# Kernel tuning notes

Measured on AMD Instinct MI355X. Metric: run time of the kernel, lower is better.

## Reference

```python
import jax, jax.numpy as jnp
import numpy as np

E = 512   # embed_size
H = 8     # heads
D = E // H
WIN = 256 # window_size
N = 4     # batch
S = 2048  # seq len (query_len == key_len == value_len)


def setup_inputs() -> dict:
    key = jax.random.key(0)
    ks = jax.random.split(key, 8)
    s = 0.02
    inp = {
        "value": jax.random.normal(ks[0], (N, S, E), jnp.float32),
        "key":   jax.random.normal(ks[1], (N, S, E), jnp.float32),
        "query": jax.random.normal(ks[2], (N, S, E), jnp.float32),
        "mask":  jnp.ones((N, 1, 1, S), jnp.int32),
        # nn.Linear params: y = x @ W.T + b, W shape [out, in]
        "Wv": jax.random.normal(ks[3], (E, E), jnp.float32) * s,
        "bv": jnp.zeros((E,), jnp.float32),
        "Wk": jax.random.normal(ks[4], (E, E), jnp.float32) * s,
        "bk": jnp.zeros((E,), jnp.float32),
        "Wq": jax.random.normal(ks[5], (E, E), jnp.float32) * s,
        "bq": jnp.zeros((E,), jnp.float32),
        "Wo": jax.random.normal(ks[6], (E, E), jnp.float32) * s,
        "bo": jnp.zeros((E,), jnp.float32),
    }
    return inp


def reference(value, key, query, mask, Wv, bv, Wk, bk, Wq, bq, Wo, bo):
    n, q_len, _ = query.shape
    k_len = key.shape[1]
    w = min(WIN, k_len)  # window_size = min(self.window_size, key_len)

    v = (value @ Wv.T + bv).reshape(n, k_len, H, D)
    k = (key   @ Wk.T + bk).reshape(n, k_len, H, D)
    q = (query @ Wq.T + bq).reshape(n, q_len, H, D)

    # Full QK scores; banded window selected below. Position j is inside the
    # window of query i iff  i - w//2 <= j <= i + w//2 (matches the torch
    # per-i slice [max(0,i-w//2), min(k_len, i+w//2+1)) ).
    scores = jnp.einsum('nqhd,nkhd->nhqk', q, k)  # [N,H,Q,K]
    ii = jnp.arange(q_len)[:, None]
    jj = jnp.arange(k_len)[None, :]
    in_win = (jj >= ii - w // 2) & (jj <= ii + w // 2)  # [Q,K]

    # Inside window: scores, masked to -inf where mask == 0.
    # Outside window: entries stay 0 (the torch code zero-inits attention).
    neg_inf = jnp.float32(-jnp.inf)
    banded = jnp.where(mask != 0, scores, neg_inf)          # broadcast [N,1,1,K]
    att_logits = jnp.where(in_win[None, None], banded, 0.0)  # [N,H,Q,K]

    att_logits = att_logits / jnp.sqrt(jnp.float32(E))  # scale by sqrt(embed_size)
    attention = jax.nn.softmax(att_logits, axis=3)

    out = jnp.einsum('nhqk,nkhd->nqhd', attention, v).reshape(n, q_len, E)
    out = out @ Wo.T + bo
    return (out, attention)
```

## Files before the change

### kernel.cpp

```cpp
#include <hip/hip_runtime.h>


typedef unsigned short u16;
typedef __bf16 bf16x8 __attribute__((ext_vector_type(8)));
typedef float  f32x4  __attribute__((ext_vector_type(4)));
typedef u16    u16x8  __attribute__((ext_vector_type(8)));

#define GLOAD_LDS(gsrc, ldst)                                                  \
    __builtin_amdgcn_global_load_lds(                                          \
        (const __attribute__((address_space(1))) void*)(gsrc),                 \
        (__attribute__((address_space(3))) void*)(ldst), 16, 0, 0)

__device__ __forceinline__ u16 f2bf(float f) {
    union { float f; unsigned u; } x; x.f = f;
    unsigned u = x.u;
    u += 0x7fffu + ((u >> 16) & 1u);
    return (u16)(u >> 16);
}

struct CvtWArgs {
    const float* src[4];
    u16*         dst[4];
};

__global__ __launch_bounds__(256) void cvt_w(CvtWArgs a) {
    int t = blockIdx.x >> 8, blk = blockIdx.x & 255;
    int i = (blk * 256 + threadIdx.x) * 4;
    float4 v = *(const float4*)(a.src[t] + i);
    ushort4 o;
    o.x = f2bf(v.x); o.y = f2bf(v.y); o.z = f2bf(v.z); o.w = f2bf(v.w);
    *(ushort4*)(a.dst[t] + i) = o;
}

__global__ __launch_bounds__(256) void gemm_qkv(
    const float* __restrict__ A0, const float* __restrict__ A1, const float* __restrict__ A2,
    const u16* __restrict__ B,
    const float* __restrict__ b0, const float* __restrict__ b1, const float* __restrict__ b2,
    u16* __restrict__ o0, u16* __restrict__ o1, u16* __restrict__ o2,
    float* __restrict__ sumv)
{
    __shared__ __attribute__((aligned(16))) u16 As[128 * 64];
    __shared__ __attribute__((aligned(16))) u16 Bs[128 * 64];

    const int tid  = threadIdx.x;
    const int lane = tid & 63;
    const int w    = tid >> 6;
    const int bm   = blockIdx.x, bn = blockIdx.y;
    const int wm   = w >> 1, wn = w & 1;

    const int t = bn >> 2;
    const float* A = (t == 0) ? A0 : (t == 1) ? A1 : A2;
    const float* Ag = A + (size_t)bm * 128 * 512;
    const u16* Bg = B + (size_t)bn * 128 * 512;

    f32x4 acc[4][4];
#pragma unroll
    for (int m = 0; m < 4; ++m)
#pragma unroll
        for (int n = 0; n < 4; ++n) acc[m][n] = 0;

    const int swc = ((lane & 7) ^ (lane >> 3)) * 8;
    const int arow = tid >> 1, ahalf = tid & 1;
    const float* asrc = Ag + (size_t)arow * 512 + ahalf * 32;

    for (int k0 = 0; k0 < 512; k0 += 64) {
        float4 fv[8];
#pragma unroll
        for (int i = 0; i < 8; ++i) fv[i] = *(const float4*)(asrc + k0 + i * 4);
#pragma unroll
        for (int c4 = 0; c4 < 4; ++c4) {
            bf16x8 pk;
#pragma unroll
            for (int e = 0; e < 8; ++e) {
                float f = ((const float*)&fv[c4 * 2])[e];
                pk[e] = (__bf16)f;
            }
            int ch = ahalf * 4 + c4;
            *(bf16x8*)(As + arow * 64 + ((ch ^ (arow & 7)) * 8)) = pk;
        }
#pragma unroll
        for (int i = 0; i < 4; ++i) {
            int g = i * 4 + w;
            GLOAD_LDS(Bg + (size_t)(g * 8 + (lane >> 3)) * 512 + k0 + swc, Bs + g * 512);
        }
        __syncthreads();

#pragma unroll
        for (int s = 0; s < 2; ++s) {
            bf16x8 af[4], bf[4];
            int c = s * 4 + (lane >> 4);
#pragma unroll
            for (int m = 0; m < 4; ++m) {
                int r = wm * 64 + m * 16 + (lane & 15);
                af[m] = *(const bf16x8*)(As + r * 64 + ((c ^ (r & 7)) * 8));
                int r2 = wn * 64 + m * 16 + (lane & 15);
                bf[m] = *(const bf16x8*)(Bs + r2 * 64 + ((c ^ (r2 & 7)) * 8));
            }
#pragma unroll
            for (int m = 0; m < 4; ++m)
#pragma unroll
                for (int n = 0; n < 4; ++n)
                    acc[m][n] = __builtin_amdgcn_mfma_f32_16x16x32_bf16(af[m], bf[n], acc[m][n], 0, 0, 0);
        }
        __syncthreads();
    }

    const float* bias = (t == 0) ? b0 : (t == 1) ? b1 : b2;
    u16* ob = (t == 0) ? o0 : (t == 1) ? o1 : o2;
    const int clbase = (bn & 3) * 128;

#pragma unroll
    for (int m = 0; m < 4; ++m) {
#pragma unroll
        for (int n = 0; n < 4; ++n) {
            int cl = clbase + wn * 64 + n * 16 + (lane & 15);
            float bb = bias[cl];
#pragma unroll
            for (int reg = 0; reg < 4; ++reg) {
                int row = bm * 128 + wm * 64 + m * 16 + (lane >> 4) * 4 + reg;
                ob[(size_t)row * 512 + cl] = f2bf(acc[m][n][reg] + bb);
            }
        }
    }

    if (t == 2) {
        int nb = bm >> 4;
#pragma unroll
        for (int n = 0; n < 4; ++n) {
            float s = 0.f;
#pragma unroll
            for (int m = 0; m < 4; ++m)
#pragma unroll
                for (int reg = 0; reg < 4; ++reg) s += acc[m][n][reg];
            s += __shfl_xor(s, 16, 64);
            s += __shfl_xor(s, 32, 64);
            if (lane < 16) {
                int cl = clbase + wn * 64 + n * 16 + lane;
                atomicAdd(sumv + nb * 512 + cl, s);
            }
        }
    }
}

__global__ __launch_bounds__(256) void gemm_o(
    const u16* __restrict__ A, const u16* __restrict__ B,
    const float* __restrict__ bias, float* __restrict__ fo)
{
    __shared__ __attribute__((aligned(16))) u16 As[128 * 64];
    __shared__ __attribute__((aligned(16))) u16 Bs[64 * 64];

    const int tid  = threadIdx.x;
    const int lane = tid & 63;
    const int w    = tid >> 6;
    const int bm   = blockIdx.x, bn = blockIdx.y;
    const int wm   = w >> 1, wn = w & 1;

    const u16* Ag = A + (size_t)bm * 128 * 512;
    const u16* Bg = B + (size_t)bn * 64 * 512;

    f32x4 acc[4][2];
#pragma unroll
    for (int m = 0; m < 4; ++m) { acc[m][0] = 0; acc[m][1] = 0; }

    const int swc = ((lane & 7) ^ (lane >> 3)) * 8;

    for (int k0 = 0; k0 < 512; k0 += 64) {
#pragma unroll
        for (int i = 0; i < 4; ++i) {
            int g = i * 4 + w;
            GLOAD_LDS(Ag + (size_t)(g * 8 + (lane >> 3)) * 512 + k0 + swc, As + g * 512);
        }
#pragma unroll
        for (int i = 0; i < 2; ++i) {
            int g = i * 4 + w;
            GLOAD_LDS(Bg + (size_t)(g * 8 + (lane >> 3)) * 512 + k0 + swc, Bs + g * 512);
        }
        __syncthreads();

#pragma unroll
        for (int s = 0; s < 2; ++s) {
            bf16x8 af[4], bf[2];
            int c = s * 4 + (lane >> 4);
#pragma unroll
            for (int m = 0; m < 4; ++m) {
                int r = wm * 64 + m * 16 + (lane & 15);
                af[m] = *(const bf16x8*)(As + r * 64 + ((c ^ (r & 7)) * 8));
            }
#pragma unroll
            for (int n = 0; n < 2; ++n) {
                int r2 = wn * 32 + n * 16 + (lane & 15);
                bf[n] = *(const bf16x8*)(Bs + r2 * 64 + ((c ^ (r2 & 7)) * 8));
            }
#pragma unroll
            for (int m = 0; m < 4; ++m)
#pragma unroll
                for (int n = 0; n < 2; ++n)
                    acc[m][n] = __builtin_amdgcn_mfma_f32_16x16x32_bf16(af[m], bf[n], acc[m][n], 0, 0, 0);
        }
        __syncthreads();
    }

#pragma unroll
    for (int m = 0; m < 4; ++m) {
#pragma unroll
        for (int n = 0; n < 2; ++n) {
            int cl = bn * 64 + wn * 32 + n * 16 + (lane & 15);
            float bb = bias[cl];
#pragma unroll
            for (int reg = 0; reg < 4; ++reg) {
                int row = bm * 128 + wm * 64 + m * 16 + (lane >> 4) * 4 + reg;
                fo[(size_t)row * 512 + cl] = acc[m][n][reg] + bb;
            }
        }
    }
}

__global__ __launch_bounds__(256) void attn_kernel(
    const u16* __restrict__ qb, const u16* __restrict__ kb,
    const u16* __restrict__ vb, const int* __restrict__ mask,
    const float* __restrict__ sumv, float* __restrict__ att,
    u16* __restrict__ oh) {
    __shared__ __attribute__((aligned(16))) char lds[79616];
    u16*   Qs      = (u16*)lds;
    float* stat_m  = (float*)lds;
    float* stat_rd = (float*)(lds + 128);
    float* stat_c  = (float*)(lds + 256);
    float* red     = (float*)(lds + 384);
    float* red2    = (float*)(lds + 640);
    u16*   Ks      = (u16*)(lds + 4096);
    float* Ab32    = (float*)(lds + 4096);
    u16*   Vt      = (u16*)(lds + 4096 + 37632);

    const int tid  = threadIdx.x;
    const int lane = tid & 63;
    const int w    = tid >> 6;
    const int bid0 = blockIdx.x;
    const int bid  = (bid0 & 7) * 256 + (bid0 >> 3);
    const int tile = bid & 63;
    const int h    = (bid >> 6) & 7;
    const int n    = bid >> 9;
    const int i0   = tile * 32;
    const int jlo  = max(0, i0 - 128);
    const float scale = 0.04419417382415922f;

    const size_t base_nh = (size_t)n * 2048 * 512 + h * 64;
    const int lr = lane >> 3;
    const int swg = ((lane & 7) ^ lr) * 8;

    GLOAD_LDS(qb + base_nh + (size_t)(i0 + w * 8 + lr) * 512 + swg, Qs + w * 512);
    for (int p = 0; p < 9; ++p) {
        int g = p * 4 + w;
        int j = min(jlo + g * 8 + lr, 2047);
        GLOAD_LDS(kb + base_nh + (size_t)j * 512 + swg, Ks + g * 512);
    }
    for (int p = 0; p < 9; ++p) {
        int idx = p * 256 + tid;
        int jj = idx >> 3, ch = idx & 7;
        int j = jlo + jj;
        u16x8 tmp = {0, 0, 0, 0, 0, 0, 0, 0};
        if (j < 2048) tmp = *(const u16x8*)(vb + base_nh + (size_t)j * 512 + ch * 8);
        int jc = jj >> 3, jr = jj & 7;
        int pjc = (jc < 32) ? (jc ^ ch) : jc;
#pragma unroll
        for (int r = 0; r < 8; ++r)
            Vt[(ch * 8 + r) * 296 + pjc * 8 + jr] = tmp[r];
    }
    __syncthreads();

    const int rbase = (w & 1) * 16;
    const int cbase = (w >> 1) * 144;
    f32x4 acc[9];
#pragma unroll
    for (int f = 0; f < 9; ++f) acc[f] = 0;

    bf16x8 aq[2];
    {
        int r = rbase + (lane & 15);
#pragma unroll
        for (int ks = 0; ks < 2; ++ks) {
            int kc = ks * 4 + (lane >> 4);
            aq[ks] = *(const bf16x8*)(Qs + r * 64 + ((kc ^ (r & 7)) * 8));
        }
    }
#pragma unroll
    for (int f = 0; f < 9; ++f) {
        int jj = cbase + f * 16 + (lane & 15);
#pragma unroll
        for (int ks = 0; ks < 2; ++ks) {
            int kc = ks * 4 + (lane >> 4);
            bf16x8 bk_ = *(const bf16x8*)(Ks + jj * 64 + ((kc ^ (jj & 7)) * 8));
            acc[f] = __builtin_amdgcn_mfma_f32_16x16x32_bf16(aq[ks], bk_, acc[f], 0, 0, 0);
        }
    }
    __syncthreads();

    const int rowg = (lane >> 4) * 4;
    f32x4 lv[9];
    float mx[4] = {-__builtin_inff(), -__builtin_inff(), -__builtin_inff(), -__builtin_inff()};
#pragma unroll
    for (int f = 0; f < 9; ++f) {
        int jj = cbase + f * 16 + (lane & 15);
        int j = jlo + jj;
        int mk = (j < 2048) ? mask[n * 2048 + j] : 0;
#pragma unroll
        for (int reg = 0; reg < 4; ++reg) {
            int i = i0 + rbase + rowg + reg;
            bool inw = (j >= i - 128) && (j <= i + 128) && (j < 2048);
            float val = (inw && mk != 0) ? acc[f][reg] * scale : -__builtin_inff();
            lv[f][reg] = val;
            mx[reg] = fmaxf(mx[reg], val);
        }
    }
#pragma unroll
    for (int mskk = 1; mskk < 16; mskk <<= 1)
#pragma unroll
        for (int reg = 0; reg < 4; ++reg)
            mx[reg] = fmaxf(mx[reg], __shfl_xor(mx[reg], mskk, 64));
    if ((lane & 15) == 0) {
#pragma unroll
        for (int reg = 0; reg < 4; ++reg) red[w * 16 + rowg + reg] = mx[reg];
    }
    __syncthreads();
    if (tid < 32) {
        int r = tid;
        int wa = (r < 16) ? 0 : 1, rr = r & 15;
        stat_m[r] = fmaxf(fmaxf(red[wa * 16 + rr], red[(wa + 2) * 16 + rr]), 0.0f);
    }
    __syncthreads();

    float m4[4];
#pragma unroll
    for (int reg = 0; reg < 4; ++reg) m4[reg] = stat_m[rbase + rowg + reg];
    float sm[4] = {0, 0, 0, 0};
#pragma unroll
    for (int f = 0; f < 9; ++f)
#pragma unroll
        for (int reg = 0; reg < 4; ++reg)
            sm[reg] += __expf(lv[f][reg] - m4[reg]);
#pragma unroll
    for (int mskk = 1; mskk < 16; mskk <<= 1)
#pragma unroll
        for (int reg = 0; reg < 4; ++reg)
            sm[reg] += __shfl_xor(sm[reg], mskk, 64);
    if ((lane & 15) == 0) {
#pragma unroll
        for (int reg = 0; reg < 4; ++reg) red2[w * 16 + rowg + reg] = sm[reg];
    }
    __syncthreads();
    if (tid < 32) {
        int r = tid, gi = i0 + r;
        int wa = (r < 16) ? 0 : 1, rr = r & 15;
        float s = red2[wa * 16 + rr] + red2[(wa + 2) * 16 + rr];
        int lo = max(0, gi - 128), hi = min(2048, gi + 129);
        float em = __expf(-stat_m[r]);
        float denom = s + (float)(2048 - (hi - lo)) * em;
        float rd = 1.0f / denom;
        stat_rd[r] = rd;
        stat_c[r] = em * rd;
    }
    __syncthreads();

    float rd4[4], c4[4];
#pragma unroll
    for (int reg = 0; reg < 4; ++reg) {
        rd4[reg] = stat_rd[rbase + rowg + reg];
        c4[reg] = stat_c[rbase + rowg + reg];
    }
#pragma unroll
    for (int f = 0; f < 9; ++f) {
        int jj = cbase + f * 16 + (lane & 15);
        int j = jlo + jj;
#pragma unroll
        for (int reg = 0; reg < 4; ++reg) {
            int it = rbase + rowg + reg;
            int i = i0 + it;
            bool inw = (j >= i - 128) && (j <= i + 128) && (j < 2048);
            float e = __expf(lv[f][reg] - m4[reg]);
            Ab32[it * 292 + jj] = inw ? (e * rd4[reg] - c4[reg]) : 0.0f;
        }
    }
    __syncthreads();

    const int rb2 = (w & 1) * 16;
    const int db  = (w >> 1) * 32;
    f32x4 po[2];
    po[0] = 0; po[1] = 0;
#pragma unroll
    for (int ks = 0; ks < 9; ++ks) {
        int kc = ks * 4 + (lane >> 4);
        int it = rb2 + (lane & 15);
        const float* ap = Ab32 + it * 292 + kc * 8;
        float4 alo = *(const float4*)(ap);
        float4 ahi = *(const float4*)(ap + 4);
        bf16x8 af;
        af[0] = (__bf16)alo.x; af[1] = (__bf16)alo.y;
        af[2] = (__bf16)alo.z; af[3] = (__bf16)alo.w;
        af[4] = (__bf16)ahi.x; af[5] = (__bf16)ahi.y;
        af[6] = (__bf16)ahi.z; af[7] = (__bf16)ahi.w;
#pragma unroll
        for (int f = 0; f < 2; ++f) {
            int d = db + f * 16 + (lane & 15);
            int phys = (kc < 32) ? (kc ^ (d >> 3)) : kc;
            bf16x8 bv_ = *(const bf16x8*)(Vt + d * 296 + phys * 8);
            po[f] = __builtin_amdgcn_mfma_f32_16x16x32_bf16(af, bv_, po[f], 0, 0, 0);
        }
    }
    {
        const float* svp = sumv + (size_t)n * 512 + h * 64;
#pragma unroll
        for (int f = 0; f < 2; ++f) {
            int d = db + f * 16 + (lane & 15);
            float sv = svp[d];
#pragma unroll
            for (int reg = 0; reg < 4; ++reg) {
                int it = rb2 + rowg + reg;
                float val = po[f][reg] + stat_c[it] * sv;
                oh[base_nh + (size_t)(i0 + it) * 512 + d] = f2bf(val);
            }
        }
    }

    {
        int jend = min(2048, jlo + 288);
        size_t rowbase = ((size_t)(n * 8 + h) * 2048 + i0) * 2048;
        for (int idx = tid; idx < 32 * 512; idx += 256) {
            int r = idx >> 9, j4 = idx & 511;
            int j = j4 * 4;
            float c = stat_c[r];
            f32x4 v = {c, c, c, c};
            if (j >= jlo && j < jend) {
                const float* ap = Ab32 + r * 292 + (j - jlo);
                v[0] += ap[0]; v[1] += ap[1]; v[2] += ap[2]; v[3] += ap[3];
            }
            __builtin_nontemporal_store(v, (f32x4*)(att + rowbase + (size_t)r * 2048 + j));
        }
    }
}

extern "C" void kernel_launch(void* const* d_in, const int* in_sizes, int n_in,
                              void* d_out, int out_size, void* d_ws, size_t ws_size,
                              hipStream_t stream) {
    const float* value = (const float*)d_in[0];
    const float* key_  = (const float*)d_in[1];
    const float* query = (const float*)d_in[2];
    const int*   mask  = (const int*)d_in[3];
    const float* Wv = (const float*)d_in[4];
    const float* bv = (const float*)d_in[5];
    const float* Wk = (const float*)d_in[6];
    const float* bk = (const float*)d_in[7];
    const float* Wq = (const float*)d_in[8];
    const float* bq = (const float*)d_in[9];
    const float* Wo = (const float*)d_in[10];
    const float* bo = (const float*)d_in[11];

    char* ws = (char*)d_ws;
    size_t off = 0;
    auto carve = [&](size_t bytes) -> char* {
        char* p = ws + off;
        off += (bytes + 255) & ~(size_t)255;
        return p;
    };
    const size_t XB = (size_t)8192 * 512 * 2;
    const size_t WB = (size_t)512 * 512 * 2;
    u16* wqkv = (u16*)carve(3 * WB);
    u16* wob  = (u16*)carve(WB);
    u16* qb   = (u16*)carve(XB);
    u16* kb   = (u16*)carve(XB);
    u16* vb2  = (u16*)carve(XB);
    u16* ohb  = (u16*)carve(XB);
    float* sumv = (float*)carve(2048 * sizeof(float));

    (void)hipMemsetAsync(sumv, 0, 2048 * sizeof(float), stream);

    CvtWArgs ca;
    ca.src[0] = Wq; ca.dst[0] = wqkv;
    ca.src[1] = Wk; ca.dst[1] = wqkv + (size_t)512 * 512;
    ca.src[2] = Wv; ca.dst[2] = wqkv + (size_t)1024 * 512;
    ca.src[3] = Wo; ca.dst[3] = wob;

    cvt_w<<<dim3(1024), 256, 0, stream>>>(ca);
    gemm_qkv<<<dim3(64, 12), 256, 0, stream>>>(
        query, key_, value, wqkv, bq, bk, bv, qb, kb, vb2, sumv);

    float* att = (float*)d_out + (size_t)4 * 2048 * 512;
    attn_kernel<<<dim3(2048), 256, 0, stream>>>(qb, kb, vb2, mask, sumv, att, ohb);
    gemm_o<<<dim3(64, 8), 256, 0, stream>>>(ohb, wob, bo, (float*)d_out);
}
```

Baseline: 643.6 us.

## Prefetch A tiles in QKV GEMM, split attention-probability stores, fold memset into cvt

The QKV GEMM now reads the next fp32 A tile into registers while MFMAs run on the current tile, and the global loads are laid out in a coalesced row-group pattern. In the attention kernel, the constant out-of-window probability writes are issued as soon as the row stats are known, before the PV matmul, and only the in-window band is written from LDS afterwards. This overlaps the large store traffic with compute. The separate hipMemsetAsync of sumv is folded into the weight-conversion kernel, removing one launch, at the cost of extra register pressure from the prefetch buffer.

```diff
diff --git a/kernel.cpp b/kernel.cpp
--- a/kernel.cpp
+++ b/kernel.cpp
@@ -23,13 +23,16 @@
     u16*         dst[4];
 };
 
-__global__ __launch_bounds__(256) void cvt_w(CvtWArgs a) {
+__global__ __launch_bounds__(256) void cvt_w(CvtWArgs a, float* __restrict__ sumv) {
     int t = blockIdx.x >> 8, blk = blockIdx.x & 255;
     int i = (blk * 256 + threadIdx.x) * 4;
     float4 v = *(const float4*)(a.src[t] + i);
     ushort4 o;
     o.x = f2bf(v.x); o.y = f2bf(v.y); o.z = f2bf(v.z); o.w = f2bf(v.w);
     *(ushort4*)(a.dst[t] + i) = o;
+    if (blockIdx.x == 0) {
+        for (int k = threadIdx.x; k < 2048; k += 256) sumv[k] = 0.f;
+    }
 }
 
 __global__ __launch_bounds__(256) void gemm_qkv(
@@ -60,23 +63,24 @@
         for (int n = 0; n < 4; ++n) acc[m][n] = 0;
 
     const int swc = ((lane & 7) ^ (lane >> 3)) * 8;
-    const int arow = tid >> 1, ahalf = tid & 1;
-    const float* asrc = Ag + (size_t)arow * 512 + ahalf * 32;
+    const int arow_g  = tid >> 4;
+    const int alane16 = tid & 15;
+    const int ach  = alane16 >> 1;
+    const int ahalf = alane16 & 1;
+
+    float4 av[8];
+#pragma unroll
+    for (int p = 0; p < 8; ++p)
+        av[p] = *(const float4*)(Ag + (size_t)(p * 16 + arow_g) * 512 + alane16 * 4);
 
     for (int k0 = 0; k0 < 512; k0 += 64) {
-        float4 fv[8];
-#pragma unroll
-        for (int i = 0; i < 8; ++i) fv[i] = *(const float4*)(asrc + k0 + i * 4);
-#pragma unroll
-        for (int c4 = 0; c4 < 4; ++c4) {
-            bf16x8 pk;
-#pragma unroll
-            for (int e = 0; e < 8; ++e) {
-                float f = ((const float*)&fv[c4 * 2])[e];
-                pk[e] = (__bf16)f;
-            }
-            int ch = ahalf * 4 + c4;
-            *(bf16x8*)(As + arow * 64 + ((ch ^ (arow & 7)) * 8)) = pk;
+#pragma unroll
+        for (int p = 0; p < 8; ++p) {
+            int row = p * 16 + arow_g;
+            ushort4 pk;
+            pk.x = f2bf(av[p].x); pk.y = f2bf(av[p].y);
+            pk.z = f2bf(av[p].z); pk.w = f2bf(av[p].w);
+            *(ushort4*)(As + row * 64 + ((ach ^ (row & 7)) * 8) + ahalf * 4) = pk;
         }
 #pragma unroll
         for (int i = 0; i < 4; ++i) {
@@ -84,6 +88,12 @@
             GLOAD_LDS(Bg + (size_t)(g * 8 + (lane >> 3)) * 512 + k0 + swc, Bs + g * 512);
         }
         __syncthreads();
+
+        if (k0 < 448) {
+#pragma unroll
+            for (int p = 0; p < 8; ++p)
+                av[p] = *(const float4*)(Ag + (size_t)(p * 16 + arow_g) * 512 + (k0 + 64) + alane16 * 4);
+        }
 
 #pragma unroll
         for (int s = 0; s < 2; ++s) {
@@ -241,9 +251,11 @@
     const int n    = bid >> 9;
     const int i0   = tile * 32;
     const int jlo  = max(0, i0 - 128);
+    const int jend = min(2048, jlo + 288);
     const float scale = 0.04419417382415922f;
 
     const size_t base_nh = (size_t)n * 2048 * 512 + h * 64;
+    const size_t rowbase = ((size_t)(n * 8 + h) * 2048 + i0) * 2048;
     const int lr = lane >> 3;
     const int swg = ((lane & 7) ^ lr) * 8;
 
@@ -359,6 +371,17 @@
         stat_c[r] = em * rd;
     }
     __syncthreads();
+
+    {
+        int j4lo = jlo >> 2, j4end = jend >> 2;
+        for (int idx = tid; idx < 32 * 512; idx += 256) {
+            int r = idx >> 9, j4 = idx & 511;
+            if (j4 >= j4lo && j4 < j4end) continue;
+            float c = stat_c[r];
+            f32x4 v = {c, c, c, c};
+            __builtin_nontemporal_store(v, (f32x4*)(att + rowbase + (size_t)r * 2048 + j4 * 4));
+        }
+    }
 
     float rd4[4], c4[4];
 #pragma unroll
@@ -405,6 +428,19 @@
             po[f] = __builtin_amdgcn_mfma_f32_16x16x32_bf16(af, bv_, po[f], 0, 0, 0);
         }
     }
+
+    {
+        int nseg = (jend - jlo) >> 2;
+        for (int idx = tid; idx < 32 * 72; idx += 256) {
+            int r = idx / 72, q = idx % 72;
+            if (q >= nseg) continue;
+            float c = stat_c[r];
+            const float* ap = Ab32 + r * 292 + q * 4;
+            f32x4 v = {ap[0] + c, ap[1] + c, ap[2] + c, ap[3] + c};
+            __builtin_nontemporal_store(v, (f32x4*)(att + rowbase + (size_t)r * 2048 + jlo + q * 4));
+        }
+    }
+
     {
         const float* svp = sumv + (size_t)n * 512 + h * 64;
 #pragma unroll
@@ -417,22 +453,6 @@
                 float val = po[f][reg] + stat_c[it] * sv;
                 oh[base_nh + (size_t)(i0 + it) * 512 + d] = f2bf(val);
             }
-        }
-    }
-
-    {
-        int jend = min(2048, jlo + 288);
-        size_t rowbase = ((size_t)(n * 8 + h) * 2048 + i0) * 2048;
-        for (int idx = tid; idx < 32 * 512; idx += 256) {
-            int r = idx >> 9, j4 = idx & 511;
-            int j = j4 * 4;
-            float c = stat_c[r];
-            f32x4 v = {c, c, c, c};
-            if (j >= jlo && j < jend) {
-                const float* ap = Ab32 + r * 292 + (j - jlo);
-                v[0] += ap[0]; v[1] += ap[1]; v[2] += ap[2]; v[3] += ap[3];
-            }
-            __builtin_nontemporal_store(v, (f32x4*)(att + rowbase + (size_t)r * 2048 + j));
         }
     }
 }
@@ -470,15 +490,13 @@
     u16* ohb  = (u16*)carve(XB);
     float* sumv = (float*)carve(2048 * sizeof(float));
 
-    (void)hipMemsetAsync(sumv, 0, 2048 * sizeof(float), stream);
-
     CvtWArgs ca;
     ca.src[0] = Wq; ca.dst[0] = wqkv;
     ca.src[1] = Wk; ca.dst[1] = wqkv + (size_t)512 * 512;
     ca.src[2] = Wv; ca.dst[2] = wqkv + (size_t)1024 * 512;
     ca.src[3] = Wo; ca.dst[3] = wob;
 
-    cvt_w<<<dim3(1024), 256, 0, stream>>>(ca);
+    cvt_w<<<dim3(1024), 256, 0, stream>>>(ca, sumv);
     gemm_qkv<<<dim3(64, 12), 256, 0, stream>>>(
         query, key_, value, wqkv, bq, bk, bv, qb, kb, vb2, sumv);
 
```

Result: no change. 631.9 us (-1.8%).
